# Optimization experiments

Measured on AMD Instinct MI355X. Metric: run time of the kernel, lower is better.

Reference implementation:

```python
import jax, jax.numpy as jnp
import numpy as np

WIRES = 4
LAYERS = 3
B = 1024
P = 14 * 14  # 196 patches


def setup_inputs() -> dict:
    key = jax.random.key(0)
    k1, k2, k3 = jax.random.split(key, 3)
    x = jax.random.uniform(k1, (B, 1, 28, 28), jnp.float32)
    q_params = jax.random.normal(k2, (LAYERS, WIRES), jnp.float32)
    W = jax.random.normal(k3, (10, 4 * 14 * 14), jnp.float32) * 0.02
    b = jnp.zeros((10,), jnp.float32)
    return {"x": x, "q_params": q_params, "W": W, "b": b}


def _cnot(state, ctrl, tgt):
    # state: [B,P,2,2,2,2]; wire w lives on axis 2+w
    c_ax, t_ax = 2 + ctrl, 2 + tgt
    s0, s1 = jnp.split(state, 2, axis=c_ax)
    s1 = jnp.flip(s1, axis=t_ax)  # flip target when control=1
    return jnp.concatenate([s0, s1], axis=c_ax)


def _circuit(xp, q_params):
    # xp: [B,P,4] RX angles per wire. Returns <Z_w> per wire: [B,P,4].
    Bn, Pn = xp.shape[0], xp.shape[1]
    state = jnp.zeros((Bn, Pn, 2, 2, 2, 2), jnp.complex64).at[:, :, 0, 0, 0, 0].set(1.0)
    for i in range(LAYERS):
        # RX(x[w]) on each wire (angle varies per batch/patch)
        for w in range(WIRES):
            half = xp[:, :, w] * 0.5
            c = jnp.cos(half).astype(jnp.complex64)
            s = (-1j) * jnp.sin(half).astype(jnp.complex64)
            mat = jnp.stack([jnp.stack([c, s], -1), jnp.stack([s, c], -1)], -2)  # [B,P,2,2]
            st = jnp.moveaxis(state, 2 + w, -1)
            st = jnp.einsum('BPij,BPuvwj->BPuvwi', mat, st)
            state = jnp.moveaxis(st, -1, 2 + w)
        state = _cnot(state, 0, 1)
        state = _cnot(state, 2, 3)
        # RZ(params[i,w]) on each wire (scalar phase, diagonal gate)
        for w in range(WIRES):
            phi = q_params[i, w].astype(jnp.complex64)
            ph = jnp.stack([jnp.exp(-0.5j * phi), jnp.exp(0.5j * phi)])  # [2]
            st = jnp.moveaxis(state, 2 + w, -1) * ph
            state = jnp.moveaxis(st, -1, 2 + w)
    probs = state.real ** 2 + state.imag ** 2  # [B,P,2,2,2,2]
    zs = []
    for w in range(WIRES):
        axes = tuple(a for a in range(2, 6) if a != 2 + w)
        m = probs.sum(axes)  # [B,P,2]
        zs.append(m[..., 0] - m[..., 1])
    return jnp.stack(zs, -1)  # [B,P,4]


def reference(x, q_params, W, b):
    Bn = x.shape[0]
    # 2x2 patches in row-major (r,c) order; per-patch flatten order matches
    # view of x[:,0,r:r+2,c:c+2]: [tl, tr, bl, br]
    xp = x[:, 0].reshape(Bn, 14, 2, 14, 2).transpose(0, 1, 3, 2, 4).reshape(Bn, P, 4)
    z = _circuit(xp, q_params)            # [B,196,4]
    feats = z.reshape(Bn, P * 4).astype(jnp.float32)  # cat order: patch-major, wire-minor
    logits = feats @ W.T + b
    return jax.nn.log_softmax(logits, axis=-1)
```

## Files before the change

kernel.cpp:

```cpp
#include <hip/hip_runtime.h>
#include <math.h>

#define WIRES   4
#define LAYERS  3
#define PATCHES 196

__global__ __launch_bounds__(256) void quanv_fused(
    const float* __restrict__ x,
    const float* __restrict__ qp,
    const float* __restrict__ Wt,
    const float* __restrict__ bias,
    float* __restrict__ out)
{
    __shared__ float feats[PATCHES * 4];
    __shared__ float phr[LAYERS][16];
    __shared__ float phim[LAYERS][16];
    __shared__ float wsum[4][10];
    __shared__ float lg[10];
    __shared__ float lse;

    const int b = blockIdx.x;
    const int t = threadIdx.x;

    if (t < LAYERS * 16) {
        const int l = t >> 4, idx = t & 15;
        float th = 0.f;
        #pragma unroll
        for (int w = 0; w < 4; ++w) {
            const float sgn = ((idx >> (3 - w)) & 1) ? 0.5f : -0.5f;
            th += sgn * qp[l * 4 + w];
        }
        float s, c;
        __sincosf(th, &s, &c);
        phr[l][idx]  = c;
        phim[l][idx] = s;
    }
    __syncthreads();

    if (t < PATCHES) {
        const int r = t / 14, cc = t % 14;
        const float* xb = x + b * 784;
        float ang[4];
        ang[0] = xb[(2 * r) * 28 + 2 * cc];
        ang[1] = xb[(2 * r) * 28 + 2 * cc + 1];
        ang[2] = xb[(2 * r + 1) * 28 + 2 * cc];
        ang[3] = xb[(2 * r + 1) * 28 + 2 * cc + 1];

        float cw[4], sw[4];
        #pragma unroll
        for (int w = 0; w < 4; ++w) __sincosf(0.5f * ang[w], &sw[w], &cw[w]);

        float sr[16], si[16];
        #pragma unroll
        for (int i = 0; i < 16; ++i) { sr[i] = 0.f; si[i] = 0.f; }
        sr[0] = 1.f;

        #pragma unroll
        for (int l = 0; l < LAYERS; ++l) {
            #pragma unroll
            for (int w = 0; w < 4; ++w) {
                const int m = 8 >> w;
                const float c = cw[w], s = sw[w];
                #pragma unroll
                for (int i = 0; i < 16; ++i) {
                    if (i & m) continue;
                    const int j = i | m;
                    const float a0r = sr[i], a0i = si[i];
                    const float a1r = sr[j], a1i = si[j];
                    sr[i] = fmaf(c, a0r,  s * a1i);
                    si[i] = fmaf(c, a0i, -s * a1r);
                    sr[j] = fmaf(c, a1r,  s * a0i);
                    si[j] = fmaf(c, a1i, -s * a0r);
                }
            }
            #pragma unroll
            for (int i = 0; i < 16; ++i) {
                if ((i & 8) && !(i & 4)) {
                    const int j = i ^ 4;
                    float tr = sr[i]; sr[i] = sr[j]; sr[j] = tr;
                    float ti = si[i]; si[i] = si[j]; si[j] = ti;
                }
            }
            #pragma unroll
            for (int i = 0; i < 16; ++i) {
                if ((i & 2) && !(i & 1)) {
                    const int j = i ^ 1;
                    float tr = sr[i]; sr[i] = sr[j]; sr[j] = tr;
                    float ti = si[i]; si[i] = si[j]; si[j] = ti;
                }
            }
            #pragma unroll
            for (int i = 0; i < 16; ++i) {
                const float pr = phr[l][i], pi = phim[l][i];
                const float rr = sr[i], ii = si[i];
                sr[i] = rr * pr - ii * pi;
                si[i] = rr * pi + ii * pr;
            }
        }

        float z[4] = {0.f, 0.f, 0.f, 0.f};
        #pragma unroll
        for (int i = 0; i < 16; ++i) {
            const float p = sr[i] * sr[i] + si[i] * si[i];
            #pragma unroll
            for (int w = 0; w < 4; ++w)
                z[w] += ((i >> (3 - w)) & 1) ? -p : p;
        }
        #pragma unroll
        for (int w = 0; w < 4; ++w) feats[t * 4 + w] = z[w];
    }
    __syncthreads();

    float part[10];
    #pragma unroll
    for (int k = 0; k < 10; ++k) part[k] = 0.f;
    for (int j = t; j < PATCHES * 4; j += 256) {
        const float f = feats[j];
        #pragma unroll
        for (int k = 0; k < 10; ++k) part[k] = fmaf(f, Wt[k * 784 + j], part[k]);
    }
    #pragma unroll
    for (int k = 0; k < 10; ++k) {
        #pragma unroll
        for (int off = 32; off > 0; off >>= 1)
            part[k] += __shfl_down(part[k], off, 64);
    }
    const int wave = t >> 6, lane = t & 63;
    if (lane == 0) {
        #pragma unroll
        for (int k = 0; k < 10; ++k) wsum[wave][k] = part[k];
    }
    __syncthreads();
    if (t < 10)
        lg[t] = bias[t] + wsum[0][t] + wsum[1][t] + wsum[2][t] + wsum[3][t];
    __syncthreads();
    if (t == 0) {
        float mx = lg[0];
        #pragma unroll
        for (int k = 1; k < 10; ++k) mx = fmaxf(mx, lg[k]);
        float se = 0.f;
        #pragma unroll
        for (int k = 0; k < 10; ++k) se += expf(lg[k] - mx);
        lse = mx + logf(se);
    }
    __syncthreads();
    if (t < 10) out[b * 10 + t] = lg[t] - lse;
}

extern "C" void kernel_launch(void* const* d_in, const int* in_sizes, int n_in,
                              void* d_out, int out_size, void* d_ws, size_t ws_size,
                              hipStream_t stream) {
    const float* x    = (const float*)d_in[0];
    const float* qp   = (const float*)d_in[1];
    const float* W    = (const float*)d_in[2];
    const float* bias = (const float*)d_in[3];
    float* out = (float*)d_out;

    const int B = in_sizes[0] / 784;
    quanv_fused<<<B, 256, 0, stream>>>(x, qp, W, bias, out);
}
```

Measured before the change: 69.05 us.

## Compute first circuit layer in closed form and stage input via shared memory

Starting from |0000>, the first RX layer yields a product state, so the kernel now builds that state directly from cos/sin products, folding in the (-i)^popcount phase, the CNOT permutation and the RZ phases. This removes one of three layers of butterfly gate work per patch. The image is also loaded with coalesced float4 reads into shared memory before the patches gather their values. The phase table setup moves to otherwise idle threads, and the final sync plus log-sum-exp broadcast is replaced by each of the ten threads computing it redundantly.

```diff
diff --git a/kernel.cpp b/kernel.cpp
--- a/kernel.cpp
+++ b/kernel.cpp
@@ -12,18 +12,23 @@
     const float* __restrict__ bias,
     float* __restrict__ out)
 {
+    __shared__ float xs[784];
     __shared__ float feats[PATCHES * 4];
     __shared__ float phr[LAYERS][16];
     __shared__ float phim[LAYERS][16];
     __shared__ float wsum[4][10];
     __shared__ float lg[10];
-    __shared__ float lse;
 
     const int b = blockIdx.x;
     const int t = threadIdx.x;
 
-    if (t < LAYERS * 16) {
-        const int l = t >> 4, idx = t & 15;
+    if (t < PATCHES) {
+        reinterpret_cast<float4*>(xs)[t] =
+            reinterpret_cast<const float4*>(x + (size_t)b * 784)[t];
+    }
+    if (t >= 208 && t < 208 + LAYERS * 16) {
+        const int idx16 = t - 208;
+        const int l = idx16 >> 4, idx = idx16 & 15;
         float th = 0.f;
         #pragma unroll
         for (int w = 0; w < 4; ++w) {
@@ -39,24 +44,44 @@
 
     if (t < PATCHES) {
         const int r = t / 14, cc = t % 14;
-        const float* xb = x + b * 784;
-        float ang[4];
-        ang[0] = xb[(2 * r) * 28 + 2 * cc];
-        ang[1] = xb[(2 * r) * 28 + 2 * cc + 1];
-        ang[2] = xb[(2 * r + 1) * 28 + 2 * cc];
-        ang[3] = xb[(2 * r + 1) * 28 + 2 * cc + 1];
+        float cw[4], sw[4];
+        {
+            const float a0 = xs[(2 * r) * 28 + 2 * cc];
+            const float a1 = xs[(2 * r) * 28 + 2 * cc + 1];
+            const float a2 = xs[(2 * r + 1) * 28 + 2 * cc];
+            const float a3 = xs[(2 * r + 1) * 28 + 2 * cc + 1];
+            __sincosf(0.5f * a0, &sw[0], &cw[0]);
+            __sincosf(0.5f * a1, &sw[1], &cw[1]);
+            __sincosf(0.5f * a2, &sw[2], &cw[2]);
+            __sincosf(0.5f * a3, &sw[3], &cw[3]);
+        }
 
-        float cw[4], sw[4];
-        #pragma unroll
-        for (int w = 0; w < 4; ++w) __sincosf(0.5f * ang[w], &sw[w], &cw[w]);
+        float m01[4], m23[4];
+        m01[0] = cw[0] * cw[1]; m01[1] = cw[0] * sw[1];
+        m01[2] = sw[0] * cw[1]; m01[3] = sw[0] * sw[1];
+        m23[0] = cw[2] * cw[3]; m23[1] = cw[2] * sw[3];
+        m23[2] = sw[2] * cw[3]; m23[3] = sw[2] * sw[3];
 
         float sr[16], si[16];
         #pragma unroll
-        for (int i = 0; i < 16; ++i) { sr[i] = 0.f; si[i] = 0.f; }
-        sr[0] = 1.f;
+        for (int i = 0; i < 16; ++i) {
+            const float m = m01[i >> 2] * m23[i & 3];
+            int ti = (i & 8) ? (i ^ 4) : i;
+            ti = (ti & 2) ? (ti ^ 1) : ti;
+            const int pc = ((i >> 3) & 1) + ((i >> 2) & 1) + ((i >> 1) & 1) + (i & 1);
+            const float pr = phr[0][ti], pi = phim[0][ti];
+            float rr, ii;
+            switch (pc & 3) {
+                case 0: rr =  m * pr; ii =  m * pi; break;
+                case 1: rr =  m * pi; ii = -m * pr; break;
+                case 2: rr = -m * pr; ii = -m * pi; break;
+                default:rr = -m * pi; ii =  m * pr; break;
+            }
+            sr[ti] = rr; si[ti] = ii;
+        }
 
         #pragma unroll
-        for (int l = 0; l < LAYERS; ++l) {
+        for (int l = 1; l < LAYERS; ++l) {
             #pragma unroll
             for (int w = 0; w < 4; ++w) {
                 const int m = 8 >> w;
@@ -78,7 +103,7 @@
                 if ((i & 8) && !(i & 4)) {
                     const int j = i ^ 4;
                     float tr = sr[i]; sr[i] = sr[j]; sr[j] = tr;
-                    float ti = si[i]; si[i] = si[j]; si[j] = ti;
+                    float ti2 = si[i]; si[i] = si[j]; si[j] = ti2;
                 }
             }
             #pragma unroll
@@ -86,7 +111,7 @@
                 if ((i & 2) && !(i & 1)) {
                     const int j = i ^ 1;
                     float tr = sr[i]; sr[i] = sr[j]; sr[j] = tr;
-                    float ti = si[i]; si[i] = si[j]; si[j] = ti;
+                    float ti2 = si[i]; si[i] = si[j]; si[j] = ti2;
                 }
             }
             #pragma unroll
@@ -101,7 +126,7 @@
         float z[4] = {0.f, 0.f, 0.f, 0.f};
         #pragma unroll
         for (int i = 0; i < 16; ++i) {
-            const float p = sr[i] * sr[i] + si[i] * si[i];
+            const float p = fmaf(sr[i], sr[i], si[i] * si[i]);
             #pragma unroll
             for (int w = 0; w < 4; ++w)
                 z[w] += ((i >> (3 - w)) & 1) ? -p : p;
@@ -134,17 +159,15 @@
     if (t < 10)
         lg[t] = bias[t] + wsum[0][t] + wsum[1][t] + wsum[2][t] + wsum[3][t];
     __syncthreads();
-    if (t == 0) {
+    if (t < 10) {
         float mx = lg[0];
         #pragma unroll
         for (int k = 1; k < 10; ++k) mx = fmaxf(mx, lg[k]);
         float se = 0.f;
         #pragma unroll
         for (int k = 0; k < 10; ++k) se += expf(lg[k] - mx);
-        lse = mx + logf(se);
+        out[b * 10 + t] = lg[t] - (mx + logf(se));
     }
-    __syncthreads();
-    if (t < 10) out[b * 10 + t] = lg[t] - lse;
 }
 
 extern "C" void kernel_launch(void* const* d_in, const int* in_sizes, int n_in,
```

New measurement: 68.28 us. No clear change (-1.1%).
